# Kernel tuning notes

Measured on AMD Instinct MI355X. Metric: run time of the kernel, lower is better.

Reference implementation:

```python
import jax, jax.numpy as jnp
import numpy as np

B, T, D = 4, 4096, 1024
HD = 64              # head_dim
H = D // HD          # n_heads = 16
C = 64               # chunk_size (T % C == 0)


def setup_inputs() -> dict:
    key = jax.random.key(0)
    k1, k2, k3 = jax.random.split(key, 3)
    out = jax.random.normal(k1, (B, T, D), jnp.float32)
    # Linear(d_model, d_model, bias=False) weights, ~1/sqrt(D) scale
    W_write = jax.random.normal(k2, (D, D), jnp.float32) * 0.03
    W_read = jax.random.normal(k3, (D, D), jnp.float32) * 0.03
    decay = jnp.full((H,), 4.6, jnp.float32)                 # torch init value
    log_alpha = jnp.log(jnp.full((H,), 0.03, jnp.float32))   # memory_alpha=0.03
    return {"out": out, "W_write": W_write, "W_read": W_read,
            "decay": decay, "log_alpha": log_alpha}


def reference(out, W_write, W_read, decay, log_alpha):
    Bb, Tt, Dd = out.shape
    d, Hh, Cc = HD, D // HD, C
    out32 = out.astype(jnp.float32)
    gamma = jax.nn.sigmoid(decay)          # (H,)
    log_gamma = jnp.log(gamma)

    # projections and head split: (B, H, T, d)
    v = (out32 @ W_write.T).reshape(Bb, Tt, Hh, d).transpose(0, 2, 1, 3)
    rk = out32.reshape(Bb, Tt, Hh, d).transpose(0, 2, 1, 3)
    wk = jnp.pad(rk[:, :, :-1], ((0, 0), (0, 0), (1, 0), (0, 0)))  # shift right by 1

    BH = Bb * Hh
    gamma_bh = jnp.tile(gamma, Bb)          # (BH,) index b*H+h -> gamma[h]
    log_gamma_bh = jnp.tile(log_gamma, Bb)
    nC = Tt // Cc
    # (nC, BH, C, d) so lax.scan runs over chunks
    v_ch = v.reshape(BH, nC, Cc, d).transpose(1, 0, 2, 3)
    rk_ch = rk.reshape(BH, nC, Cc, d).transpose(1, 0, 2, 3)
    wk_ch = wk.reshape(BH, nC, Cc, d).transpose(1, 0, 2, 3)

    p = jnp.arange(Cc)
    diffs = jnp.clip(p[:, None] - 1 - p[None, :], 0)          # (C, C)
    causal = p[:, None] > p[None, :]
    # per-(b,h) intra-chunk decay mask (BH, C, C)
    M = jnp.exp(diffs[None].astype(jnp.float32) * log_gamma_bh[:, None, None]) * causal[None]
    g_p = gamma_bh[:, None] ** p[None, :].astype(jnp.float32)            # (BH, C)
    g_w = gamma_bh[:, None] ** (Cc - 1 - p)[None, :].astype(jnp.float32)  # (BH, C)
    g_C = gamma_bh ** Cc                                                  # (BH,)

    def scan_fn(W, chunk):
        rk_c, wk_c, v_c = chunk                                   # each (BH, C, d)
        inter = jnp.einsum('bij,bcj->bci', W, rk_c) * g_p[:, :, None]
        S = jnp.einsum('bcd,bkd->bck', rk_c, wk_c)                # (BH, C, C)
        intra = jnp.einsum('bck,bkd->bcd', S * M, v_c)
        W_new = g_C[:, None, None] * W + jnp.einsum('bci,bcj->bij', v_c * g_w[:, :, None], wk_c)
        return W_new, inter + intra

    W0 = jnp.zeros((BH, d, d), jnp.float32)
    _, reads = jax.lax.scan(scan_fn, W0, (rk_ch, wk_ch, v_ch))   # (nC, BH, C, d)
    reads = reads.transpose(1, 0, 2, 3).reshape(Bb, Hh, Tt, d)
    alpha = jnp.exp(log_alpha)[None, :, None, None]
    reads = (alpha * reads).transpose(0, 2, 1, 3).reshape(Bb, Tt, Dd)
    return out + (reads @ W_read.T).astype(out.dtype)
```

## Files before the change

kernel.cpp:

```cpp
#include <hip/hip_runtime.h>
#include <hip/hip_bf16.h>
#include <stdint.h>


typedef __bf16 bf16x8 __attribute__((ext_vector_type(8)));
typedef float f32x4 __attribute__((ext_vector_type(4)));

#define GAS __attribute__((address_space(1)))
#define LAS __attribute__((address_space(3)))

__device__ __forceinline__ unsigned short f2bf(float f) {
  unsigned u = __float_as_uint(f);
  u = (u + 0x7fffu + ((u >> 16) & 1u)) >> 16;
  return (unsigned short)u;
}
__device__ __forceinline__ float bf2f(unsigned short h) {
  return __uint_as_float(((unsigned)h) << 16);
}

__global__ __launch_bounds__(256) void cast_f32_to_bf16(
    const float* __restrict__ src, unsigned short* __restrict__ dst, int n8) {
  int i = blockIdx.x * 256 + threadIdx.x;
  if (i >= n8) return;
  const float4* s = (const float4*)src + (size_t)i * 2;
  float4 f0 = s[0], f1 = s[1];
  union { uint4 u4; unsigned short us[8]; } o;
  o.us[0] = f2bf(f0.x); o.us[1] = f2bf(f0.y); o.us[2] = f2bf(f0.z); o.us[3] = f2bf(f0.w);
  o.us[4] = f2bf(f1.x); o.us[5] = f2bf(f1.y); o.us[6] = f2bf(f1.z); o.us[7] = f2bf(f1.w);
  ((uint4*)dst)[i] = o.u4;
}

__global__ __launch_bounds__(256) void cast_weights(
    const float* __restrict__ w1, const float* __restrict__ w2,
    unsigned short* __restrict__ dst) {
  int i = blockIdx.x * 256 + threadIdx.x;
  const float* src = (i < 131072) ? w1 : w2;
  int j = (i < 131072) ? i : i - 131072;
  const float4* s = (const float4*)src + (size_t)j * 2;
  float4 f0 = s[0], f1 = s[1];
  union { uint4 u4; unsigned short us[8]; } o;
  o.us[0] = f2bf(f0.x); o.us[1] = f2bf(f0.y); o.us[2] = f2bf(f0.z); o.us[3] = f2bf(f0.w);
  o.us[4] = f2bf(f1.x); o.us[5] = f2bf(f1.y); o.us[6] = f2bf(f1.z); o.us[7] = f2bf(f1.w);
  ((uint4*)dst)[i] = o.u4;
}


#define STG(XB, SLOT, HIDX, HF, KT)                                                  \
  do {                                                                               \
    if ((KT) < nT) {                                                                 \
      _Pragma("unroll") for (int r_ = 0; r_ < 2; r_++)                               \
          __builtin_amdgcn_global_load_lds(                                          \
              (GAS void*)(void*)((XB) +                                              \
                                 (size_t)((HF) * 128 + (tid >> 3) + r_ * 64) * K +   \
                                 ((KT) << 6) + srcc),                                \
              (LAS void*)(&lds[SLOT][HIDX][w64 * 512 + r_ * 4096]), 16, 0, 0);       \
    }                                                                                \
  } while (0)

#define DSRA(SLOT, MH)                                                               \
  _Pragma("unroll") for (int m_ = 0; m_ < 4; m_++)                                   \
  _Pragma("unroll") for (int ks_ = 0; ks_ < 2; ks_++)                                \
      a[m_][ks_] = *(const bf16x8*)&lds[SLOT][aH][((MH) * 64 + m_ * 16 + lm) * 64 +  \
                                                  ((ks_ * 32 + q4 * 8) ^ swz)];

#define DSRB(SLOT, BB, N0)                                                           \
  _Pragma("unroll") for (int n_ = 0; n_ < 2; n_++)                                   \
  _Pragma("unroll") for (int ks_ = 0; ks_ < 2; ks_++)                                \
      BB[n_][ks_] = *(const bf16x8*)&lds[SLOT][bH][(brow0 + ((N0) + n_) * 16 + lm) * 64 + \
                                                   ((ks_ * 32 + q4 * 8) ^ swz)];

#define MMA(MH, BB, N0)                                                              \
  __builtin_amdgcn_s_setprio(1);                                                     \
  _Pragma("unroll") for (int m_ = 0; m_ < 4; m_++)                                   \
  _Pragma("unroll") for (int n_ = 0; n_ < 2; n_++)                                   \
  _Pragma("unroll") for (int ks_ = 0; ks_ < 2; ks_++)                                \
      acc[(MH) * 4 + m_][(N0) + n_] = __builtin_amdgcn_mfma_f32_16x16x32_bf16(       \
          a[m_][ks_], BB[n_][ks_], acc[(MH) * 4 + m_][(N0) + n_], 0, 0, 0);          \
  __builtin_amdgcn_s_setprio(0);

#define BARW                                                                         \
  __builtin_amdgcn_s_barrier();                                                      \
  asm volatile("s_waitcnt lgkmcnt(0)" ::: "memory");                                 \
  __builtin_amdgcn_sched_barrier(0);

#define BARE                                                                         \
  __builtin_amdgcn_s_barrier();                                                      \
  __builtin_amdgcn_sched_barrier(0);

template <bool ADD>
__global__ __launch_bounds__(512, 2) void gemm256(
    const unsigned short* __restrict__ A, const unsigned short* __restrict__ B,
    const unsigned short* __restrict__ base_bf, void* __restrict__ Cout,
    int M, int N, int K) {
  __shared__ unsigned short lds[2][4][8192];
  int tid = threadIdx.x;
  int l = tid & 63, w64 = tid >> 6;
  int lm = l & 15, q4 = l >> 4;
  int swz = ((lm >> 2) & 1) << 5;
  int srcc = ((tid & 7) * 8) ^ (((tid >> 5) & 1) << 5);
  int aH = w64 >> 2;
  int bH = 2 + ((w64 & 3) >> 1);
  int brow0 = (w64 & 1) * 64;
  int id = blockIdx.x;
  int xcd = id & 7, s = id >> 3;
  int bn = s & 3, bm = (s >> 2) * 8 + xcd;
  const unsigned short* Ab = A + (size_t)bm * 256 * K;
  const unsigned short* Bb = B + (size_t)bn * 256 * K;
  const int nT = K >> 6, nI = nT >> 1;

  STG(Bb, 0, 2, 0, 0); STG(Bb, 0, 3, 1, 0);
  STG(Ab, 0, 0, 0, 0); STG(Ab, 0, 1, 1, 0);
  STG(Bb, 1, 2, 0, 1); STG(Bb, 1, 3, 1, 1);
  asm volatile("s_waitcnt vmcnt(4)" ::: "memory");
  __builtin_amdgcn_s_barrier();
  __builtin_amdgcn_sched_barrier(0);

  f32x4 acc[8][4];
  if constexpr (ADD) {
#pragma unroll
    for (int mh = 0; mh < 2; mh++)
#pragma unroll
      for (int m = 0; m < 4; m++)
#pragma unroll
        for (int nf = 0; nf < 4; nf++) {
          int r0 = bm * 256 + (w64 >> 2) * 128 + mh * 64 + m * 16 + q4 * 4;
          int col = bn * 256 + (w64 & 3) * 64 + nf * 16 + lm;
#pragma unroll
          for (int j = 0; j < 4; j++)
            acc[mh * 4 + m][nf][j] = bf2f(base_bf[(size_t)(r0 + j) * N + col]);
        }
  } else {
#pragma unroll
    for (int mf = 0; mf < 8; mf++)
#pragma unroll
      for (int nf = 0; nf < 4; nf++) acc[mf][nf] = (f32x4){0.f, 0.f, 0.f, 0.f};
  }

  bf16x8 a[4][2], b0[2][2], b1[2][2];
  for (int i = 0; i < nI; i++) {
    int t1 = 2 * i + 1, t2 = 2 * i + 2, t3 = 2 * i + 3;
    DSRA(0, 0); DSRB(0, b0, 0); STG(Ab, 1, 0, 0, t1);
    BARW; MMA(0, b0, 0); BARE;
    DSRB(0, b1, 2); STG(Ab, 1, 1, 1, t1);
    BARW; MMA(0, b1, 2); BARE;
    DSRA(0, 1); STG(Bb, 0, 2, 0, t2);
    BARW; MMA(1, b1, 2); BARE;
    STG(Bb, 0, 3, 1, t2);
    BARW; MMA(1, b0, 0);
    if (i < nI - 1) { asm volatile("s_waitcnt vmcnt(4)" ::: "memory"); }
    else            { asm volatile("s_waitcnt vmcnt(0)" ::: "memory"); }
    BARE;
    DSRA(1, 0); DSRB(1, b0, 0); STG(Ab, 0, 0, 0, t2);
    BARW; MMA(0, b0, 0); BARE;
    DSRB(1, b1, 2); STG(Ab, 0, 1, 1, t2);
    BARW; MMA(0, b1, 2); BARE;
    DSRA(1, 1); STG(Bb, 1, 2, 0, t3);
    BARW; MMA(1, b1, 2); BARE;
    STG(Bb, 1, 3, 1, t3);
    BARW; MMA(1, b0, 0);
    if (i < nI - 1) { asm volatile("s_waitcnt vmcnt(4)" ::: "memory"); }
    BARE;
  }

#pragma unroll
  for (int mh = 0; mh < 2; mh++)
#pragma unroll
    for (int m = 0; m < 4; m++)
#pragma unroll
      for (int nf = 0; nf < 4; nf++) {
        int r0 = bm * 256 + (w64 >> 2) * 128 + mh * 64 + m * 16 + q4 * 4;
        int col = bn * 256 + (w64 & 3) * 64 + nf * 16 + lm;
#pragma unroll
        for (int j = 0; j < 4; j++) {
          if constexpr (ADD)
            ((float*)Cout)[(size_t)(r0 + j) * N + col] = acc[mh * 4 + m][nf][j];
          else
            ((unsigned short*)Cout)[(size_t)(r0 + j) * N + col] = f2bf(acc[mh * 4 + m][nf][j]);
        }
      }
}

__global__ __launch_bounds__(256) void chunk_local(
    const unsigned short* __restrict__ rkg,
    const unsigned short* __restrict__ vg,
    const float* __restrict__ decay,
    unsigned short* __restrict__ intra_bf,
    unsigned short* __restrict__ U_bf) {
  int c = blockIdx.x, bh = blockIdx.y;
  int b = bh >> 4, h = bh & 15;
  int tid = threadIdx.x, l = tid & 63, w = tid >> 6;
  float gamma = 1.0f / (1.0f + __expf(-decay[h]));
  float lg = __logf(gamma);

  __shared__ unsigned short rk_s[64 * 72];
  __shared__ unsigned short wk_s[64 * 72];
  __shared__ unsigned short wkT_s[64 * 72];
  __shared__ unsigned short vT_s[64 * 72];
  __shared__ unsigned short S_s[64 * 72];

  const size_t rowbase = (((size_t)b * 4096 + (size_t)c * 64) * 1024) + h * 64;

#pragma unroll
  for (int r = 0; r < 2; r++) {
    int e = r * 256 + tid;
    int p = e >> 3, seg = e & 7;
    uint4 dr = *(const uint4*)(rkg + rowbase + (size_t)p * 1024 + seg * 8);
    *(uint4*)&rk_s[p * 72 + seg * 8] = dr;
    uint4 dv = *(const uint4*)(vg + rowbase + (size_t)p * 1024 + seg * 8);
    {
      unsigned uu[4] = {dv.x, dv.y, dv.z, dv.w};
#pragma unroll
      for (int qq = 0; qq < 4; qq++) {
        vT_s[(seg * 8 + qq * 2) * 72 + p] = (unsigned short)(uu[qq] & 0xffffu);
        vT_s[(seg * 8 + qq * 2 + 1) * 72 + p] = (unsigned short)(uu[qq] >> 16);
      }
    }
    int tg = c * 64 + p - 1;
    uint4 dw = make_uint4(0u, 0u, 0u, 0u);
    if (tg >= 0) dw = *(const uint4*)(rkg + ((size_t)b * 4096 + tg) * 1024 + h * 64 + seg * 8);
    *(uint4*)&wk_s[p * 72 + seg * 8] = dw;
    {
      unsigned uu[4] = {dw.x, dw.y, dw.z, dw.w};
#pragma unroll
      for (int qq = 0; qq < 4; qq++) {
        wkT_s[(seg * 8 + qq * 2) * 72 + p] = (unsigned short)(uu[qq] & 0xffffu);
        wkT_s[(seg * 8 + qq * 2 + 1) * 72 + p] = (unsigned short)(uu[qq] >> 16);
      }
    }
  }
  __syncthreads();

  int lm = l & 15, q4 = l >> 4;

  {
    bf16x8 a0 = *(const bf16x8*)&rk_s[(w * 16 + lm) * 72 + q4 * 8];
    bf16x8 a1 = *(const bf16x8*)&rk_s[(w * 16 + lm) * 72 + 32 + q4 * 8];
#pragma unroll
    for (int ni = 0; ni < 4; ni++) {
      bf16x8 b0 = *(const bf16x8*)&wk_s[(ni * 16 + lm) * 72 + q4 * 8];
      bf16x8 b1 = *(const bf16x8*)&wk_s[(ni * 16 + lm) * 72 + 32 + q4 * 8];
      f32x4 acc = {0.f, 0.f, 0.f, 0.f};
      acc = __builtin_amdgcn_mfma_f32_16x16x32_bf16(a0, b0, acc, 0, 0, 0);
      acc = __builtin_amdgcn_mfma_f32_16x16x32_bf16(a1, b1, acc, 0, 0, 0);
#pragma unroll
      for (int j = 0; j < 4; j++) {
        int p = w * 16 + q4 * 4 + j;
        int q = ni * 16 + lm;
        float m = (p > q) ? __expf(lg * (float)(p - 1 - q)) : 0.0f;
        S_s[p * 72 + q] = f2bf(acc[j] * m);
      }
    }
  }
  __syncthreads();

  {
    bf16x8 a0 = *(const bf16x8*)&S_s[(w * 16 + lm) * 72 + q4 * 8];
    bf16x8 a1 = *(const bf16x8*)&S_s[(w * 16 + lm) * 72 + 32 + q4 * 8];
#pragma unroll
    for (int ni = 0; ni < 4; ni++) {
      bf16x8 b0 = *(const bf16x8*)&vT_s[(ni * 16 + lm) * 72 + q4 * 8];
      bf16x8 b1 = *(const bf16x8*)&vT_s[(ni * 16 + lm) * 72 + 32 + q4 * 8];
      f32x4 acc = {0.f, 0.f, 0.f, 0.f};
      acc = __builtin_amdgcn_mfma_f32_16x16x32_bf16(a0, b0, acc, 0, 0, 0);
      acc = __builtin_amdgcn_mfma_f32_16x16x32_bf16(a1, b1, acc, 0, 0, 0);
#pragma unroll
      for (int j = 0; j < 4; j++) {
        int p = w * 16 + q4 * 4 + j;
        int i = ni * 16 + lm;
        intra_bf[rowbase + (size_t)p * 1024 + i] = f2bf(acc[j]);
      }
    }
  }

  {
    bf16x8 a0 = *(const bf16x8*)&vT_s[(w * 16 + lm) * 72 + q4 * 8];
    bf16x8 a1 = *(const bf16x8*)&vT_s[(w * 16 + lm) * 72 + 32 + q4 * 8];
#pragma unroll
    for (int jj = 0; jj < 8; jj++) {
      int p0 = q4 * 8 + jj;
      a0[jj] = (__bf16)((float)a0[jj] * __expf(lg * (float)(63 - p0)));
      a1[jj] = (__bf16)((float)a1[jj] * __expf(lg * (float)(63 - (p0 + 32))));
    }
    size_t ub = ((size_t)bh * 64 + c) * 4096;
#pragma unroll
    for (int nj = 0; nj < 4; nj++) {
      bf16x8 b0 = *(const bf16x8*)&wkT_s[(nj * 16 + lm) * 72 + q4 * 8];
      bf16x8 b1 = *(const bf16x8*)&wkT_s[(nj * 16 + lm) * 72 + 32 + q4 * 8];
      f32x4 acc = {0.f, 0.f, 0.f, 0.f};
      acc = __builtin_amdgcn_mfma_f32_16x16x32_bf16(a0, b0, acc, 0, 0, 0);
      acc = __builtin_amdgcn_mfma_f32_16x16x32_bf16(a1, b1, acc, 0, 0, 0);
#pragma unroll
      for (int j = 0; j < 4; j++) {
        int i = w * 16 + q4 * 4 + j;
        int col = nj * 16 + lm;
        U_bf[ub + i * 64 + col] = f2bf(acc[j]);
      }
    }
  }
}

__global__ __launch_bounds__(256) void scan_w(
    const unsigned short* __restrict__ U_bf, const float* __restrict__ decay,
    unsigned short* __restrict__ Wst) {
  int nsl = blockIdx.x, bh = blockIdx.y;
  int h = bh & 15;
  float gamma = 1.0f / (1.0f + __expf(-decay[h]));
  float gC = __expf(64.0f * __logf(gamma));
  int n0 = nsl * 512 + threadIdx.x * 2;
  const unsigned short* Ub = U_bf + (size_t)bh * 64 * 4096 + n0;
  unsigned short* Wb = Wst + (size_t)bh * 64 * 4096 + n0;
  float w0 = 0.f, w1 = 0.f;
#pragma unroll
  for (int c = 0; c < 64; c++) {
    unsigned u = *(const unsigned*)(Ub + (size_t)c * 4096);
    ushort2 sv;
    sv.x = f2bf(w0);
    sv.y = f2bf(w1);
    *(ushort2*)(Wb + (size_t)c * 4096) = sv;
    w0 = gC * w0 + bf2f((unsigned short)(u & 0xffffu));
    w1 = gC * w1 + bf2f((unsigned short)(u >> 16));
  }
}

__global__ __launch_bounds__(256) void inter_combine(
    const unsigned short* __restrict__ rkg, const unsigned short* __restrict__ Wst,
    const unsigned short* __restrict__ intra_bf,
    const float* __restrict__ decay, const float* __restrict__ log_alpha,
    unsigned short* __restrict__ reads_bf) {
  int c = blockIdx.x, bh = blockIdx.y;
  int b = bh >> 4, h = bh & 15;
  int tid = threadIdx.x, l = tid & 63, w = tid >> 6;
  int lm = l & 15, q4 = l >> 4;
  float gamma = 1.0f / (1.0f + __expf(-decay[h]));
  float lg = __logf(gamma);
  float alpha = __expf(log_alpha[h]);

  __shared__ unsigned short rk_s[64 * 72];
  __shared__ unsigned short W_s[64 * 72];
  __shared__ unsigned short in_s[64 * 72];

  const size_t rowbase = (((size_t)b * 4096 + (size_t)c * 64) * 1024) + h * 64;
  const size_t wbase = ((size_t)bh * 64 + c) * 4096;

#pragma unroll
  for (int r = 0; r < 2; r++) {
    int e = r * 256 + tid;
    int p = e >> 3, seg = (e & 7) * 8;
    *(uint4*)&rk_s[p * 72 + seg] = *(const uint4*)(rkg + rowbase + (size_t)p * 1024 + seg);
    *(uint4*)&in_s[p * 72 + seg] = *(const uint4*)(intra_bf + rowbase + (size_t)p * 1024 + seg);
    *(uint4*)&W_s[p * 72 + seg] = *(const uint4*)(Wst + wbase + (size_t)p * 64 + seg);
  }
  __syncthreads();

  bf16x8 a0 = *(const bf16x8*)&rk_s[(w * 16 + lm) * 72 + q4 * 8];
  bf16x8 a1 = *(const bf16x8*)&rk_s[(w * 16 + lm) * 72 + 32 + q4 * 8];
#pragma unroll
  for (int ni = 0; ni < 4; ni++) {
    bf16x8 b0 = *(const bf16x8*)&W_s[(ni * 16 + lm) * 72 + q4 * 8];
    bf16x8 b1 = *(const bf16x8*)&W_s[(ni * 16 + lm) * 72 + 32 + q4 * 8];
    f32x4 acc = {0.f, 0.f, 0.f, 0.f};
    acc = __builtin_amdgcn_mfma_f32_16x16x32_bf16(a0, b0, acc, 0, 0, 0);
    acc = __builtin_amdgcn_mfma_f32_16x16x32_bf16(a1, b1, acc, 0, 0, 0);
#pragma unroll
    for (int j = 0; j < 4; j++) {
      int p = w * 16 + q4 * 4 + j;
      int i = ni * 16 + lm;
      float gp = __expf(lg * (float)p);
      reads_bf[rowbase + (size_t)p * 1024 + i] =
          f2bf(alpha * (acc[j] * gp + bf2f(in_s[p * 72 + i])));
    }
  }
}

extern "C" void kernel_launch(void* const* d_in, const int* in_sizes, int n_in,
                              void* d_out, int out_size, void* d_ws, size_t ws_size,
                              hipStream_t stream) {
  const float* out_f = (const float*)d_in[0];
  const float* Ww = (const float*)d_in[1];
  const float* Wr = (const float*)d_in[2];
  const float* decay = (const float*)d_in[3];
  const float* lalpha = (const float*)d_in[4];

  char* ws = (char*)d_ws;
  unsigned short* outbf = (unsigned short*)(ws + 0);
  unsigned short* vbf   = (unsigned short*)(ws + 33554432);
  unsigned short* wwbf  = (unsigned short*)(ws + 67108864);
  unsigned short* wrbf  = (unsigned short*)(ws + 69206016);
  unsigned short* intra = (unsigned short*)(ws + 71303168);
  unsigned short* U     = (unsigned short*)(ws + 104857600);
  unsigned short* Wst   = (unsigned short*)(ws + 138412032);
  unsigned short* reads = (unsigned short*)(ws + 171966464);

  cast_f32_to_bf16<<<dim3(8192), 256, 0, stream>>>(out_f, outbf, 16777216 / 8);
  cast_weights<<<dim3(1024), 256, 0, stream>>>(Ww, Wr, wwbf);

  gemm256<false><<<dim3(256), 512, 0, stream>>>(outbf, wwbf, nullptr, vbf, 16384, 1024, 1024);

  chunk_local<<<dim3(64, 64), 256, 0, stream>>>(outbf, vbf, decay, intra, U);

  scan_w<<<dim3(8, 64), 256, 0, stream>>>(U, decay, Wst);
  inter_combine<<<dim3(64, 64), 256, 0, stream>>>(outbf, Wst, intra, decay, lalpha, reads);

  gemm256<true><<<dim3(256), 512, 0, stream>>>(reads, wrbf, outbf, d_out, 16384, 1024, 1024);
}
```

Before: 285.1 us.

## Merge cast kernels, share shifted-key LDS tile, tabulate decay powers, widen scan

The two f32-to-bf16 cast launches become a single kernel, which removes one launch. In chunk_local, rk and the shifted wk now share one 65-row LDS buffer, so one global load pass is dropped. Decay powers are precomputed once into a 64-entry shared table instead of calling exp per element. scan_w now processes four columns per thread with wider loads and stores over half as many blocks, which trades fewer, wider memory ops for lower parallelism in an already small grid.

```diff
diff --git a/kernel.cpp b/kernel.cpp
--- a/kernel.cpp
+++ b/kernel.cpp
@@ -18,32 +18,29 @@
   return __uint_as_float(((unsigned)h) << 16);
 }
 
-__global__ __launch_bounds__(256) void cast_f32_to_bf16(
-    const float* __restrict__ src, unsigned short* __restrict__ dst, int n8) {
+__global__ __launch_bounds__(256) void cast_all(
+    const float* __restrict__ outf, const float* __restrict__ w1,
+    const float* __restrict__ w2, unsigned short* __restrict__ outbf,
+    unsigned short* __restrict__ wbf) {
   int i = blockIdx.x * 256 + threadIdx.x;
-  if (i >= n8) return;
-  const float4* s = (const float4*)src + (size_t)i * 2;
-  float4 f0 = s[0], f1 = s[1];
-  union { uint4 u4; unsigned short us[8]; } o;
-  o.us[0] = f2bf(f0.x); o.us[1] = f2bf(f0.y); o.us[2] = f2bf(f0.z); o.us[3] = f2bf(f0.w);
-  o.us[4] = f2bf(f1.x); o.us[5] = f2bf(f1.y); o.us[6] = f2bf(f1.z); o.us[7] = f2bf(f1.w);
-  ((uint4*)dst)[i] = o.u4;
-}
-
-__global__ __launch_bounds__(256) void cast_weights(
-    const float* __restrict__ w1, const float* __restrict__ w2,
-    unsigned short* __restrict__ dst) {
-  int i = blockIdx.x * 256 + threadIdx.x;
-  const float* src = (i < 131072) ? w1 : w2;
-  int j = (i < 131072) ? i : i - 131072;
+  const float* src;
+  uint4* dst;
+  int j;
+  if (i < 2097152) {
+    src = outf; j = i; dst = (uint4*)outbf;
+  } else {
+    j = i - 2097152;
+    dst = (uint4*)wbf;
+    if (j < 131072) { src = w1; }
+    else { src = w2; j -= 131072; dst += 131072; }
+  }
   const float4* s = (const float4*)src + (size_t)j * 2;
   float4 f0 = s[0], f1 = s[1];
   union { uint4 u4; unsigned short us[8]; } o;
   o.us[0] = f2bf(f0.x); o.us[1] = f2bf(f0.y); o.us[2] = f2bf(f0.z); o.us[3] = f2bf(f0.w);
   o.us[4] = f2bf(f1.x); o.us[5] = f2bf(f1.y); o.us[6] = f2bf(f1.z); o.us[7] = f2bf(f1.w);
-  ((uint4*)dst)[i] = o.u4;
-}
-
+  dst[(i < 2097152) ? i : (i - 2097152 < 131072 ? i - 2097152 : i - 2097152 - 131072)] = o.u4;
+}
 
 #define STG(XB, SLOT, HIDX, HF, KT)                                                  \
   do {                                                                               \
@@ -192,20 +189,21 @@
   float gamma = 1.0f / (1.0f + __expf(-decay[h]));
   float lg = __logf(gamma);
 
-  __shared__ unsigned short rk_s[64 * 72];
-  __shared__ unsigned short wk_s[64 * 72];
+  __shared__ unsigned short kr_s[65 * 72];
   __shared__ unsigned short wkT_s[64 * 72];
   __shared__ unsigned short vT_s[64 * 72];
   __shared__ unsigned short S_s[64 * 72];
+  __shared__ float pw_s[64];
+
+  if (tid < 64) pw_s[tid] = __expf(lg * (float)tid);
 
   const size_t rowbase = (((size_t)b * 4096 + (size_t)c * 64) * 1024) + h * 64;
+  const size_t bb = (size_t)b * 4096;
 
 #pragma unroll
   for (int r = 0; r < 2; r++) {
     int e = r * 256 + tid;
     int p = e >> 3, seg = e & 7;
-    uint4 dr = *(const uint4*)(rkg + rowbase + (size_t)p * 1024 + seg * 8);
-    *(uint4*)&rk_s[p * 72 + seg * 8] = dr;
     uint4 dv = *(const uint4*)(vg + rowbase + (size_t)p * 1024 + seg * 8);
     {
       unsigned uu[4] = {dv.x, dv.y, dv.z, dv.w};
@@ -215,10 +213,10 @@
         vT_s[(seg * 8 + qq * 2 + 1) * 72 + p] = (unsigned short)(uu[qq] >> 16);
       }
     }
-    int tg = c * 64 + p - 1;
+    int tg = c * 64 - 1 + p;
     uint4 dw = make_uint4(0u, 0u, 0u, 0u);
-    if (tg >= 0) dw = *(const uint4*)(rkg + ((size_t)b * 4096 + tg) * 1024 + h * 64 + seg * 8);
-    *(uint4*)&wk_s[p * 72 + seg * 8] = dw;
+    if (tg >= 0) dw = *(const uint4*)(rkg + (bb + tg) * 1024 + h * 64 + seg * 8);
+    *(uint4*)&kr_s[p * 72 + seg * 8] = dw;
     {
       unsigned uu[4] = {dw.x, dw.y, dw.z, dw.w};
 #pragma unroll
@@ -228,17 +226,21 @@
       }
     }
   }
+  if (tid < 8) {
+    uint4 dw = *(const uint4*)(rkg + (bb + (size_t)c * 64 + 63) * 1024 + h * 64 + tid * 8);
+    *(uint4*)&kr_s[64 * 72 + tid * 8] = dw;
+  }
   __syncthreads();
 
   int lm = l & 15, q4 = l >> 4;
 
   {
-    bf16x8 a0 = *(const bf16x8*)&rk_s[(w * 16 + lm) * 72 + q4 * 8];
-    bf16x8 a1 = *(const bf16x8*)&rk_s[(w * 16 + lm) * 72 + 32 + q4 * 8];
+    bf16x8 a0 = *(const bf16x8*)&kr_s[(w * 16 + lm + 1) * 72 + q4 * 8];
+    bf16x8 a1 = *(const bf16x8*)&kr_s[(w * 16 + lm + 1) * 72 + 32 + q4 * 8];
 #pragma unroll
     for (int ni = 0; ni < 4; ni++) {
-      bf16x8 b0 = *(const bf16x8*)&wk_s[(ni * 16 + lm) * 72 + q4 * 8];
-      bf16x8 b1 = *(const bf16x8*)&wk_s[(ni * 16 + lm) * 72 + 32 + q4 * 8];
+      bf16x8 b0 = *(const bf16x8*)&kr_s[(ni * 16 + lm) * 72 + q4 * 8];
+      bf16x8 b1 = *(const bf16x8*)&kr_s[(ni * 16 + lm) * 72 + 32 + q4 * 8];
       f32x4 acc = {0.f, 0.f, 0.f, 0.f};
       acc = __builtin_amdgcn_mfma_f32_16x16x32_bf16(a0, b0, acc, 0, 0, 0);
       acc = __builtin_amdgcn_mfma_f32_16x16x32_bf16(a1, b1, acc, 0, 0, 0);
@@ -246,7 +248,7 @@
       for (int j = 0; j < 4; j++) {
         int p = w * 16 + q4 * 4 + j;
         int q = ni * 16 + lm;
-        float m = (p > q) ? __expf(lg * (float)(p - 1 - q)) : 0.0f;
+        float m = (p > q) ? pw_s[p - 1 - q] : 0.0f;
         S_s[p * 72 + q] = f2bf(acc[j] * m);
       }
     }
@@ -278,8 +280,8 @@
 #pragma unroll
     for (int jj = 0; jj < 8; jj++) {
       int p0 = q4 * 8 + jj;
-      a0[jj] = (__bf16)((float)a0[jj] * __expf(lg * (float)(63 - p0)));
-      a1[jj] = (__bf16)((float)a1[jj] * __expf(lg * (float)(63 - (p0 + 32))));
+      a0[jj] = (__bf16)((float)a0[jj] * pw_s[63 - p0]);
+      a1[jj] = (__bf16)((float)a1[jj] * pw_s[63 - (p0 + 32)]);
     }
     size_t ub = ((size_t)bh * 64 + c) * 4096;
 #pragma unroll
@@ -306,19 +308,20 @@
   int h = bh & 15;
   float gamma = 1.0f / (1.0f + __expf(-decay[h]));
   float gC = __expf(64.0f * __logf(gamma));
-  int n0 = nsl * 512 + threadIdx.x * 2;
+  int n0 = nsl * 1024 + threadIdx.x * 4;
   const unsigned short* Ub = U_bf + (size_t)bh * 64 * 4096 + n0;
   unsigned short* Wb = Wst + (size_t)bh * 64 * 4096 + n0;
-  float w0 = 0.f, w1 = 0.f;
+  float w0 = 0.f, w1 = 0.f, w2 = 0.f, w3 = 0.f;
 #pragma unroll
   for (int c = 0; c < 64; c++) {
-    unsigned u = *(const unsigned*)(Ub + (size_t)c * 4096);
-    ushort2 sv;
-    sv.x = f2bf(w0);
-    sv.y = f2bf(w1);
-    *(ushort2*)(Wb + (size_t)c * 4096) = sv;
-    w0 = gC * w0 + bf2f((unsigned short)(u & 0xffffu));
-    w1 = gC * w1 + bf2f((unsigned short)(u >> 16));
+    uint2 u = *(const uint2*)(Ub + (size_t)c * 4096);
+    ushort4 sv;
+    sv.x = f2bf(w0); sv.y = f2bf(w1); sv.z = f2bf(w2); sv.w = f2bf(w3);
+    *(ushort4*)(Wb + (size_t)c * 4096) = sv;
+    w0 = gC * w0 + bf2f((unsigned short)(u.x & 0xffffu));
+    w1 = gC * w1 + bf2f((unsigned short)(u.x >> 16));
+    w2 = gC * w2 + bf2f((unsigned short)(u.y & 0xffffu));
+    w3 = gC * w3 + bf2f((unsigned short)(u.y >> 16));
   }
 }
 
@@ -391,14 +394,13 @@
   unsigned short* Wst   = (unsigned short*)(ws + 138412032);
   unsigned short* reads = (unsigned short*)(ws + 171966464);
 
-  cast_f32_to_bf16<<<dim3(8192), 256, 0, stream>>>(out_f, outbf, 16777216 / 8);
-  cast_weights<<<dim3(1024), 256, 0, stream>>>(Ww, Wr, wwbf);
+  cast_all<<<dim3(9216), 256, 0, stream>>>(out_f, Ww, Wr, outbf, wwbf);
 
   gemm256<false><<<dim3(256), 512, 0, stream>>>(outbf, wwbf, nullptr, vbf, 16384, 1024, 1024);
 
   chunk_local<<<dim3(64, 64), 256, 0, stream>>>(outbf, vbf, decay, intra, U);
 
-  scan_w<<<dim3(8, 64), 256, 0, stream>>>(U, decay, Wst);
+  scan_w<<<dim3(4, 64), 256, 0, stream>>>(U, decay, Wst);
   inter_combine<<<dim3(64, 64), 256, 0, stream>>>(outbf, Wst, intra, decay, lalpha, reads);
 
   gemm256<true><<<dim3(256), 512, 0, stream>>>(reads, wrbf, outbf, d_out, 16384, 1024, 1024);
```

After: 279.6 us. No clear change (-1.9%).
